# Kernel optimization log

Measured on AMD Instinct MI355X. Metric: run time of the kernel, lower is better.

Reference implementation:

```python
import jax, jax.numpy as jnp
import numpy as np

USER_NUM = 100000
ITEM_NUM = 50000
N_NODES = USER_NUM + ITEM_NUM
EMB_DIM = 64
N_LAYERS = 3
NNZ = 4800000


def setup_inputs() -> dict:
    key = jax.random.key(0)
    k1, k2, k3, k4, k5 = jax.random.split(key, 5)
    user_emb = 0.2 * jax.random.normal(k1, (USER_NUM, EMB_DIM), dtype=jnp.float32)
    item_emb = 0.2 * jax.random.normal(k2, (ITEM_NUM, EMB_DIM), dtype=jnp.float32)
    adj_row = jax.random.randint(k3, (NNZ,), 0, N_NODES, dtype=jnp.int32)
    adj_col = jax.random.randint(k4, (NNZ,), 0, N_NODES, dtype=jnp.int32)
    adj_vals = jax.random.uniform(k5, (NNZ,), dtype=jnp.float32)
    return {
        "user_emb": user_emb,
        "item_emb": item_emb,
        "adj_row": adj_row,
        "adj_col": adj_col,
        "adj_vals": adj_vals,
    }


def _spmm(row, col, vals, x):
    # sparse [N,N] @ dense [N,D] via gather + weighted segment-sum
    msg = vals[:, None] * x[col]  # [nnz, D]
    return jax.ops.segment_sum(msg, row, num_segments=N_NODES)


def reference(user_emb, item_emb, adj_row, adj_col, adj_vals):
    ego = jnp.concatenate([user_emb, item_emb], axis=0)  # [N, D]
    acc = ego  # running sum over layers (equivalent to stack+mean)
    for _ in range(N_LAYERS):
        ego = _spmm(adj_row, adj_col, adj_vals, ego)
        acc = acc + ego
    out = acc / jnp.asarray(N_LAYERS + 1, dtype=acc.dtype)
    return out[:USER_NUM], out[USER_NUM:]
```

## Files before the change

kernel.cpp:

```cpp
#include <hip/hip_runtime.h>

#define USER_NUM 100000
#define ITEM_NUM 50000
#define N_NODES  150000
#define EMB_DIM  64
#define NNZ      4800000

#define CB_SHIFT 9
#define ROWS_PER_CB 512
#define NCB ((N_NODES + ROWS_PER_CB - 1) / ROWS_PER_CB)
#define CB_CAP 17024
#define TILE 2048
#define NTILES ((NNZ + TILE - 1) / TILE)
#define PT_THREADS 512
#define EPT (TILE / PT_THREADS)
#define CUR_STRIDE 16

__device__ __forceinline__ float bflo(unsigned u) {
    return __uint_as_float(u << 16);
}
__device__ __forceinline__ float bfhi(unsigned u) {
    return __uint_as_float(u & 0xFFFF0000u);
}
__device__ __forceinline__ unsigned f2bf(float f) {
    unsigned u = __float_as_uint(f);
    return (u + 0x7FFFu + ((u >> 16) & 1u)) >> 16;
}

__global__ void lgcn_init(const float4* __restrict__ user,
                          const float4* __restrict__ item,
                          uint4* __restrict__ xb,
                          int* __restrict__ bucket_cursor) {
    int i = blockIdx.x * blockDim.x + threadIdx.x;
    if (i < NCB) bucket_cursor[i * CUR_STRIDE] = i * CB_CAP;
    if (i >= N_NODES * 8) return;
    const int user_chunks = USER_NUM * 8;
    float4 f0, f1;
    if (i < user_chunks) {
        f0 = user[i * 2];
        f1 = user[i * 2 + 1];
    } else {
        f0 = item[(i - user_chunks) * 2];
        f1 = item[(i - user_chunks) * 2 + 1];
    }
    uint4 p;
    p.x = f2bf(f0.x) | (f2bf(f0.y) << 16);
    p.y = f2bf(f0.z) | (f2bf(f0.w) << 16);
    p.z = f2bf(f1.x) | (f2bf(f1.y) << 16);
    p.w = f2bf(f1.z) | (f2bf(f1.w) << 16);
    xb[i] = p;
}

__global__ __launch_bounds__(PT_THREADS, 8) void lgcn_partition(
    const int* __restrict__ row,
    const int* __restrict__ col,
    const float* __restrict__ vals,
    int* __restrict__ bucket_cursor,
    int2* __restrict__ t_cv) {
    __shared__ int histB[NCB];
    __shared__ int delta[NCB];
    __shared__ int2 pcv[TILE];
    __shared__ unsigned short bb[TILE];
    int* sscan = (int*)pcv;

    int tid = threadIdx.x;
    int tileStart = blockIdx.x * TILE;
    int tileCount = NNZ - tileStart;
    if (tileCount > TILE) tileCount = TILE;

    for (int b = tid; b < NCB; b += PT_THREADS) histB[b] = 0;
    __syncthreads();

    int rws[EPT];
    int lps[EPT];
#pragma unroll
    for (int k = 0; k < EPT; ++k) {
        int le = tid + k * PT_THREADS;
        int r = -1, lp = 0;
        if (le < tileCount) {
            r = row[tileStart + le];
            lp = atomicAdd(&histB[r >> CB_SHIFT], 1);
        }
        rws[k] = r;
        lps[k] = lp;
    }
    __syncthreads();

    int h = (tid < NCB) ? histB[tid] : 0;
    sscan[tid] = h;
    __syncthreads();
    for (int off = 1; off < PT_THREADS; off <<= 1) {
        int x = (tid >= off) ? sscan[tid - off] : 0;
        __syncthreads();
        sscan[tid] += x;
        __syncthreads();
    }
    int sb = 0, rb = 0;
    if (tid < NCB) {
        sb = sscan[tid] - h;
        rb = h ? atomicAdd(&bucket_cursor[tid * CUR_STRIDE], h) : 0;
    }
    __syncthreads();
    if (tid < NCB) {
        histB[tid] = sb;
        delta[tid] = rb - sb;
    }
    __syncthreads();

#pragma unroll
    for (int k = 0; k < EPT; ++k) {
        int le = tid + k * PT_THREADS;
        if (le < tileCount) {
            int e = tileStart + le;
            int cc = col[e];
            float vv = vals[e];
            int r = rws[k];
            int b = r >> CB_SHIFT;
            int slot = histB[b] + lps[k];
            pcv[slot] = make_int2(((r & (ROWS_PER_CB - 1)) << 18) | cc,
                                  __float_as_int(vv));
            bb[slot] = (unsigned short)b;
        }
    }
    __syncthreads();

#pragma unroll
    for (int k = 0; k < EPT; ++k) {
        int i = tid + k * PT_THREADS;
        if (i < tileCount) {
            int b = bb[i];
            int gpos = delta[b] + i;
            if (gpos < (b + 1) * CB_CAP)
                t_cv[gpos] = pcv[i];
        }
    }
}

__global__ __launch_bounds__(1024) void lgcn_finalize(
    const int* __restrict__ bucket_cursor,
    const int2* __restrict__ t_cv,
    int2* __restrict__ csr_cv,
    int2* __restrict__ row_se) {
    __shared__ int hist[ROWS_PER_CB];
    __shared__ int cur[ROWS_PER_CB];
    __shared__ int sscan[1024];
    int t = threadIdx.x;
    int b = blockIdx.x;

    int v = 0;
    if (t < NCB) {
        int cb = bucket_cursor[t * CUR_STRIDE] - t * CB_CAP;
        v = (cb > CB_CAP) ? CB_CAP : cb;
    }
    sscan[t] = v;
    __syncthreads();
    for (int off = 1; off < 1024; off <<= 1) {
        int x = (t >= off) ? sscan[t - off] : 0;
        __syncthreads();
        sscan[t] += x;
        __syncthreads();
    }
    int prev = (b == 0) ? 0 : sscan[b - 1];
    int bbase = prev;
    int count = sscan[b] - prev;

    int lo = b * ROWS_PER_CB;
    int nrows = N_NODES - lo;
    if (nrows > ROWS_PER_CB) nrows = ROWS_PER_CB;

    if (t < ROWS_PER_CB) hist[t] = 0;
    __syncthreads();

    int base = b * CB_CAP;
    int eEnd = base + count;
    int e = base + t;
    for (; e + 3 * 1024 < eEnd; e += 4 * 1024) {
        int2 c0 = t_cv[e];
        int2 c1 = t_cv[e + 1024];
        int2 c2 = t_cv[e + 2048];
        int2 c3 = t_cv[e + 3072];
        atomicAdd(&hist[(unsigned)c0.x >> 18], 1);
        atomicAdd(&hist[(unsigned)c1.x >> 18], 1);
        atomicAdd(&hist[(unsigned)c2.x >> 18], 1);
        atomicAdd(&hist[(unsigned)c3.x >> 18], 1);
    }
    for (; e < eEnd; e += 1024)
        atomicAdd(&hist[(unsigned)t_cv[e].x >> 18], 1);
    __syncthreads();

    int h = (t < ROWS_PER_CB) ? hist[t] : 0;
    sscan[t] = h;
    __syncthreads();
    for (int off = 1; off < 1024; off <<= 1) {
        int x = (t >= off) ? sscan[t - off] : 0;
        __syncthreads();
        sscan[t] += x;
        __syncthreads();
    }
    int p = bbase + sscan[t] - h;
    if (t < nrows) {
        row_se[lo + t] = make_int2(p, p + h);
        cur[t] = p;
    }
    __syncthreads();

    e = base + t;
    for (; e + 3 * 1024 < eEnd; e += 4 * 1024) {
        int2 c0 = t_cv[e];
        int2 c1 = t_cv[e + 1024];
        int2 c2 = t_cv[e + 2048];
        int2 c3 = t_cv[e + 3072];
        int p0 = atomicAdd(&cur[(unsigned)c0.x >> 18], 1);
        int p1 = atomicAdd(&cur[(unsigned)c1.x >> 18], 1);
        int p2 = atomicAdd(&cur[(unsigned)c2.x >> 18], 1);
        int p3 = atomicAdd(&cur[(unsigned)c3.x >> 18], 1);
        csr_cv[p0] = make_int2(c0.x & 0x3FFFF, c0.y);
        csr_cv[p1] = make_int2(c1.x & 0x3FFFF, c1.y);
        csr_cv[p2] = make_int2(c2.x & 0x3FFFF, c2.y);
        csr_cv[p3] = make_int2(c3.x & 0x3FFFF, c3.y);
    }
    for (; e < eEnd; e += 1024) {
        int2 cv = t_cv[e];
        int pos = atomicAdd(&cur[(unsigned)cv.x >> 18], 1);
        csr_cv[pos] = make_int2(cv.x & 0x3FFFF, cv.y);
    }
}

#define FMA8(vv, uu) do {                                          \
    a[0] += (vv) * bflo((uu).x); a[1] += (vv) * bfhi((uu).x);      \
    a[2] += (vv) * bflo((uu).y); a[3] += (vv) * bfhi((uu).y);      \
    a[4] += (vv) * bflo((uu).z); a[5] += (vv) * bfhi((uu).z);      \
    a[6] += (vv) * bflo((uu).w); a[7] += (vv) * bfhi((uu).w);      \
} while (0)

#define SPMM_BODY                                                  \
    int gid = blockIdx.x * blockDim.x + threadIdx.x;               \
    int r = gid >> 6;                                              \
    if (r >= N_NODES) return;                                      \
    int lane = threadIdx.x & 63;                                   \
    int c = lane & 7;                                              \
    int sub = lane >> 3;                                           \
    int2 se = row_se[r];                                           \
    int start = se.x;                                              \
    int end = se.y;                                                \
    float a[8] = {0.f, 0.f, 0.f, 0.f, 0.f, 0.f, 0.f, 0.f};         \
    int e = start + sub;                                           \
    for (; e + 24 < end; e += 32) {                                \
        int2 cv0 = csr_cv[e];                                      \
        int2 cv1 = csr_cv[e + 8];                                  \
        int2 cv2 = csr_cv[e + 16];                                 \
        int2 cv3 = csr_cv[e + 24];                                 \
        uint4 u0 = xb[cv0.x * 8 + c];                              \
        uint4 u1 = xb[cv1.x * 8 + c];                              \
        uint4 u2 = xb[cv2.x * 8 + c];                              \
        uint4 u3 = xb[cv3.x * 8 + c];                              \
        float v0 = __int_as_float(cv0.y);                          \
        float v1 = __int_as_float(cv1.y);                          \
        float v2 = __int_as_float(cv2.y);                          \
        float v3 = __int_as_float(cv3.y);                          \
        FMA8(v0, u0);                                              \
        FMA8(v1, u1);                                              \
        FMA8(v2, u2);                                              \
        FMA8(v3, u3);                                              \
    }                                                              \
    if (e + 8 < end) {                                             \
        int2 cv0 = csr_cv[e];                                      \
        int2 cv1 = csr_cv[e + 8];                                  \
        uint4 u0 = xb[cv0.x * 8 + c];                              \
        uint4 u1 = xb[cv1.x * 8 + c];                              \
        float v0 = __int_as_float(cv0.y);                          \
        float v1 = __int_as_float(cv1.y);                          \
        FMA8(v0, u0);                                              \
        FMA8(v1, u1);                                              \
        e += 16;                                                   \
    }                                                              \
    if (e < end) {                                                 \
        int2 cv = csr_cv[e];                                       \
        uint4 u = xb[cv.x * 8 + c];                                \
        float v = __int_as_float(cv.y);                            \
        FMA8(v, u);                                                \
    }                                                              \
    _Pragma("unroll")                                              \
    for (int k = 0; k < 8; ++k) {                                  \
        a[k] += __shfl_xor(a[k], 8);                               \
        a[k] += __shfl_xor(a[k], 16);                               \
        a[k] += __shfl_xor(a[k], 32);                              \
    }

__global__ __launch_bounds__(256, 8) void lgcn_spmm_bf16(
    const int2* __restrict__ row_se,
    const int2* __restrict__ csr_cv,
    const uint4* __restrict__ xb,
    uint4* __restrict__ yb) {
    SPMM_BODY
    if (sub == 0) {
        uint4 p;
        p.x = f2bf(a[0]) | (f2bf(a[1]) << 16);
        p.y = f2bf(a[2]) | (f2bf(a[3]) << 16);
        p.z = f2bf(a[4]) | (f2bf(a[5]) << 16);
        p.w = f2bf(a[6]) | (f2bf(a[7]) << 16);
        yb[r * 8 + c] = p;
    }
}

__global__ __launch_bounds__(256, 8) void lgcn_spmm_final(
    const int2* __restrict__ row_se,
    const int2* __restrict__ csr_cv,
    const uint4* __restrict__ xb,
    const uint4* __restrict__ x0b,
    const uint4* __restrict__ y1b,
    float4* __restrict__ out) {
    SPMM_BODY
    if (sub == 0) {
        uint4 q0 = x0b[r * 8 + c];
        uint4 q1 = y1b[r * 8 + c];
        uint4 q2 = xb[r * 8 + c];
        float4 o0, o1;
        o0.x = (bflo(q0.x) + bflo(q1.x) + bflo(q2.x) + a[0]) * 0.25f;
        o0.y = (bfhi(q0.x) + bfhi(q1.x) + bfhi(q2.x) + a[1]) * 0.25f;
        o0.z = (bflo(q0.y) + bflo(q1.y) + bflo(q2.y) + a[2]) * 0.25f;
        o0.w = (bfhi(q0.y) + bfhi(q1.y) + bfhi(q2.y) + a[3]) * 0.25f;
        o1.x = (bflo(q0.z) + bflo(q1.z) + bflo(q2.z) + a[4]) * 0.25f;
        o1.y = (bfhi(q0.z) + bfhi(q1.z) + bfhi(q2.z) + a[5]) * 0.25f;
        o1.z = (bflo(q0.w) + bflo(q1.w) + bflo(q2.w) + a[6]) * 0.25f;
        o1.w = (bfhi(q0.w) + bfhi(q1.w) + bfhi(q2.w) + a[7]) * 0.25f;
        int idx = r * 16 + c * 2;
        out[idx] = o0;
        out[idx + 1] = o1;
    }
}

extern "C" void kernel_launch(void* const* d_in, const int* in_sizes, int n_in,
                              void* d_out, int out_size, void* d_ws, size_t ws_size,
                              hipStream_t stream) {
    const float* user_emb = (const float*)d_in[0];
    const float* item_emb = (const float*)d_in[1];
    const int*   adj_row  = (const int*)d_in[2];
    const int*   adj_col  = (const int*)d_in[3];
    const float* adj_vals = (const float*)d_in[4];
    float* out = (float*)d_out;

    char* base = (char*)d_ws;
    uint4* xb_a   = (uint4*)base;
    int2*  csr_cv = (int2*)(base + 19200000);
    char*  S      = base + 57600000;
    const size_t T_ENTRIES = (size_t)NCB * CB_CAP;
    int2*  t_cv   = (int2*)S;
    uint4* y1b    = (uint4*)S;
    uint4* y2b    = (uint4*)(S + 19200000);
    char*  tail   = S + T_ENTRIES * 8;
    int2*  row_se = (int2*)tail;
    int*   bucket_cursor = (int*)(tail + (size_t)N_NODES * 8);

    {
        int threads = 256;
        int blocks = (N_NODES * 8 + threads - 1) / threads;
        lgcn_init<<<blocks, threads, 0, stream>>>(
            (const float4*)user_emb, (const float4*)item_emb, xb_a,
            bucket_cursor);
    }

    lgcn_partition<<<NTILES, PT_THREADS, 0, stream>>>(
        adj_row, adj_col, adj_vals, bucket_cursor, t_cv);
    lgcn_finalize<<<NCB, 1024, 0, stream>>>(
        bucket_cursor, t_cv, csr_cv, row_se);

    const int spmm_block = 256;
    const int spmm_grid = (N_NODES * 64 + spmm_block - 1) / spmm_block;
    lgcn_spmm_bf16<<<spmm_grid, spmm_block, 0, stream>>>(
        row_se, csr_cv, xb_a, y1b);
    lgcn_spmm_bf16<<<spmm_grid, spmm_block, 0, stream>>>(
        row_se, csr_cv, y1b, y2b);
    lgcn_spmm_final<<<spmm_grid, spmm_block, 0, stream>>>(
        row_se, csr_cv, y2b, xb_a, y1b, (float4*)out);
}
```

Before: 504.4 us.

## Fuse embedding init into partition kernel and single-pass finalize scatter

Folds the bf16 embedding conversion into extra blocks of the partition kernel and replaces the cursor-initialising kernel with a memset, with bucket offsets now added in the partition kernel. The finalize kernel keeps each edge and its local histogram position in registers, so it reads t_cv once instead of twice and drops the second round of shared atomics. This removes one kernel launch and one pass over the bucketed edges. In exchange it adds register pressure from the per-thread arrays of 17 entries and makes the partition grid larger.

```diff
diff --git a/kernel.cpp b/kernel.cpp
--- a/kernel.cpp
+++ b/kernel.cpp
@@ -15,6 +15,8 @@
 #define PT_THREADS 512
 #define EPT (TILE / PT_THREADS)
 #define CUR_STRIDE 16
+#define IBLK ((N_NODES * 8 + PT_THREADS - 1) / PT_THREADS)
+#define EPTF ((CB_CAP + 1023) / 1024)
 
 __device__ __forceinline__ float bflo(unsigned u) {
     return __uint_as_float(u << 16);
@@ -25,30 +27,6 @@
 __device__ __forceinline__ unsigned f2bf(float f) {
     unsigned u = __float_as_uint(f);
     return (u + 0x7FFFu + ((u >> 16) & 1u)) >> 16;
-}
-
-__global__ void lgcn_init(const float4* __restrict__ user,
-                          const float4* __restrict__ item,
-                          uint4* __restrict__ xb,
-                          int* __restrict__ bucket_cursor) {
-    int i = blockIdx.x * blockDim.x + threadIdx.x;
-    if (i < NCB) bucket_cursor[i * CUR_STRIDE] = i * CB_CAP;
-    if (i >= N_NODES * 8) return;
-    const int user_chunks = USER_NUM * 8;
-    float4 f0, f1;
-    if (i < user_chunks) {
-        f0 = user[i * 2];
-        f1 = user[i * 2 + 1];
-    } else {
-        f0 = item[(i - user_chunks) * 2];
-        f1 = item[(i - user_chunks) * 2 + 1];
-    }
-    uint4 p;
-    p.x = f2bf(f0.x) | (f2bf(f0.y) << 16);
-    p.y = f2bf(f0.z) | (f2bf(f0.w) << 16);
-    p.z = f2bf(f1.x) | (f2bf(f1.y) << 16);
-    p.w = f2bf(f1.z) | (f2bf(f1.w) << 16);
-    xb[i] = p;
 }
 
 __global__ __launch_bounds__(PT_THREADS, 8) void lgcn_partition(
@@ -56,14 +34,39 @@
     const int* __restrict__ col,
     const float* __restrict__ vals,
     int* __restrict__ bucket_cursor,
-    int2* __restrict__ t_cv) {
+    int2* __restrict__ t_cv,
+    const float4* __restrict__ user,
+    const float4* __restrict__ item,
+    uint4* __restrict__ xb) {
+    int tid = threadIdx.x;
+
+    if (blockIdx.x >= NTILES) {
+        int i = (blockIdx.x - NTILES) * PT_THREADS + tid;
+        if (i >= N_NODES * 8) return;
+        const int user_chunks = USER_NUM * 8;
+        float4 f0, f1;
+        if (i < user_chunks) {
+            f0 = user[i * 2];
+            f1 = user[i * 2 + 1];
+        } else {
+            f0 = item[(i - user_chunks) * 2];
+            f1 = item[(i - user_chunks) * 2 + 1];
+        }
+        uint4 p;
+        p.x = f2bf(f0.x) | (f2bf(f0.y) << 16);
+        p.y = f2bf(f0.z) | (f2bf(f0.w) << 16);
+        p.z = f2bf(f1.x) | (f2bf(f1.y) << 16);
+        p.w = f2bf(f1.z) | (f2bf(f1.w) << 16);
+        xb[i] = p;
+        return;
+    }
+
     __shared__ int histB[NCB];
     __shared__ int delta[NCB];
     __shared__ int2 pcv[TILE];
     __shared__ unsigned short bb[TILE];
     int* sscan = (int*)pcv;
 
-    int tid = threadIdx.x;
     int tileStart = blockIdx.x * TILE;
     int tileCount = NNZ - tileStart;
     if (tileCount > TILE) tileCount = TILE;
@@ -103,7 +106,7 @@
     __syncthreads();
     if (tid < NCB) {
         histB[tid] = sb;
-        delta[tid] = rb - sb;
+        delta[tid] = tid * CB_CAP + rb - sb;
     }
     __syncthreads();
 
@@ -142,14 +145,13 @@
     int2* __restrict__ csr_cv,
     int2* __restrict__ row_se) {
     __shared__ int hist[ROWS_PER_CB];
-    __shared__ int cur[ROWS_PER_CB];
     __shared__ int sscan[1024];
     int t = threadIdx.x;
     int b = blockIdx.x;
 
     int v = 0;
     if (t < NCB) {
-        int cb = bucket_cursor[t * CUR_STRIDE] - t * CB_CAP;
+        int cb = bucket_cursor[t * CUR_STRIDE];
         v = (cb > CB_CAP) ? CB_CAP : cb;
     }
     sscan[t] = v;
@@ -173,19 +175,19 @@
 
     int base = b * CB_CAP;
     int eEnd = base + count;
-    int e = base + t;
-    for (; e + 3 * 1024 < eEnd; e += 4 * 1024) {
-        int2 c0 = t_cv[e];
-        int2 c1 = t_cv[e + 1024];
-        int2 c2 = t_cv[e + 2048];
-        int2 c3 = t_cv[e + 3072];
-        atomicAdd(&hist[(unsigned)c0.x >> 18], 1);
-        atomicAdd(&hist[(unsigned)c1.x >> 18], 1);
-        atomicAdd(&hist[(unsigned)c2.x >> 18], 1);
-        atomicAdd(&hist[(unsigned)c3.x >> 18], 1);
-    }
-    for (; e < eEnd; e += 1024)
-        atomicAdd(&hist[(unsigned)t_cv[e].x >> 18], 1);
+    int2 cvs[EPTF];
+    int  lps[EPTF];
+#pragma unroll
+    for (int k = 0; k < EPTF; ++k) {
+        int e = base + t + k * 1024;
+        if (e < eEnd) {
+            int2 cv = t_cv[e];
+            cvs[k] = cv;
+            lps[k] = atomicAdd(&hist[(unsigned)cv.x >> 18], 1);
+        } else {
+            lps[k] = -1;
+        }
+    }
     __syncthreads();
 
     int h = (t < ROWS_PER_CB) ? hist[t] : 0;
@@ -198,31 +200,18 @@
         __syncthreads();
     }
     int p = bbase + sscan[t] - h;
-    if (t < nrows) {
-        row_se[lo + t] = make_int2(p, p + h);
-        cur[t] = p;
-    }
-    __syncthreads();
-
-    e = base + t;
-    for (; e + 3 * 1024 < eEnd; e += 4 * 1024) {
-        int2 c0 = t_cv[e];
-        int2 c1 = t_cv[e + 1024];
-        int2 c2 = t_cv[e + 2048];
-        int2 c3 = t_cv[e + 3072];
-        int p0 = atomicAdd(&cur[(unsigned)c0.x >> 18], 1);
-        int p1 = atomicAdd(&cur[(unsigned)c1.x >> 18], 1);
-        int p2 = atomicAdd(&cur[(unsigned)c2.x >> 18], 1);
-        int p3 = atomicAdd(&cur[(unsigned)c3.x >> 18], 1);
-        csr_cv[p0] = make_int2(c0.x & 0x3FFFF, c0.y);
-        csr_cv[p1] = make_int2(c1.x & 0x3FFFF, c1.y);
-        csr_cv[p2] = make_int2(c2.x & 0x3FFFF, c2.y);
-        csr_cv[p3] = make_int2(c3.x & 0x3FFFF, c3.y);
-    }
-    for (; e < eEnd; e += 1024) {
-        int2 cv = t_cv[e];
-        int pos = atomicAdd(&cur[(unsigned)cv.x >> 18], 1);
-        csr_cv[pos] = make_int2(cv.x & 0x3FFFF, cv.y);
+    if (t < nrows) row_se[lo + t] = make_int2(p, p + h);
+    __syncthreads();
+    if (t < ROWS_PER_CB) hist[t] = p;
+    __syncthreads();
+
+#pragma unroll
+    for (int k = 0; k < EPTF; ++k) {
+        if (lps[k] >= 0) {
+            int2 cv = cvs[k];
+            int pos = hist[(unsigned)cv.x >> 18] + lps[k];
+            csr_cv[pos] = make_int2(cv.x & 0x3FFFF, cv.y);
+        }
     }
 }
 
@@ -283,7 +272,7 @@
     _Pragma("unroll")                                              \
     for (int k = 0; k < 8; ++k) {                                  \
         a[k] += __shfl_xor(a[k], 8);                               \
-        a[k] += __shfl_xor(a[k], 16);                               \
+        a[k] += __shfl_xor(a[k], 16);                              \
         a[k] += __shfl_xor(a[k], 32);                              \
     }
 
@@ -352,16 +341,12 @@
     int2*  row_se = (int2*)tail;
     int*   bucket_cursor = (int*)(tail + (size_t)N_NODES * 8);
 
-    {
-        int threads = 256;
-        int blocks = (N_NODES * 8 + threads - 1) / threads;
-        lgcn_init<<<blocks, threads, 0, stream>>>(
-            (const float4*)user_emb, (const float4*)item_emb, xb_a,
-            bucket_cursor);
-    }
-
-    lgcn_partition<<<NTILES, PT_THREADS, 0, stream>>>(
-        adj_row, adj_col, adj_vals, bucket_cursor, t_cv);
+    hipMemsetAsync(bucket_cursor, 0, (size_t)NCB * CUR_STRIDE * sizeof(int),
+                   stream);
+
+    lgcn_partition<<<NTILES + IBLK, PT_THREADS, 0, stream>>>(
+        adj_row, adj_col, adj_vals, bucket_cursor, t_cv,
+        (const float4*)user_emb, (const float4*)item_emb, xb_a);
     lgcn_finalize<<<NCB, 1024, 0, stream>>>(
         bucket_cursor, t_cv, csr_cv, row_se);
 
```

Result: faster. 492.7 us (-2.3%).
